# Performance work log

Measured on AMD Instinct MI355X. Metric: run time of the kernel, lower is better.

The kernel has to match this reference:

```python
import jax, jax.numpy as jnp
import numpy as np

INPUT_DIM = 32
HIDDEN = 64
BATCH = 4096
SEQ = 256


def _uniform(key, shape, bound):
    return jax.random.uniform(key, shape, dtype=jnp.float32, minval=-bound, maxval=bound)


def setup_inputs() -> dict:
    key = jax.random.key(0)
    ks = jax.random.split(key, 16)
    kb = 1.0 / np.sqrt(HIDDEN)  # torch LSTM/Linear init bound
    x = jax.random.normal(ks[0], (BATCH, SEQ, INPUT_DIM), dtype=jnp.float32)
    # LSTM layer 0 (input_dim -> hidden), gate order i,f,g,o stacked on dim 0
    Wih0 = _uniform(ks[1], (4 * HIDDEN, INPUT_DIM), kb)
    Whh0 = _uniform(ks[2], (4 * HIDDEN, HIDDEN), kb)
    bih0 = _uniform(ks[3], (4 * HIDDEN,), kb)
    bhh0 = _uniform(ks[4], (4 * HIDDEN,), kb)
    # LSTM layer 1 (hidden -> hidden)
    Wih1 = _uniform(ks[5], (4 * HIDDEN, HIDDEN), kb)
    Whh1 = _uniform(ks[6], (4 * HIDDEN, HIDDEN), kb)
    bih1 = _uniform(ks[7], (4 * HIDDEN,), kb)
    bhh1 = _uniform(ks[8], (4 * HIDDEN,), kb)
    # MLP head
    W1 = _uniform(ks[9], (HIDDEN, HIDDEN), kb)
    b1 = _uniform(ks[10], (HIDDEN,), kb)
    W2 = _uniform(ks[11], (1, HIDDEN), kb)
    b2 = _uniform(ks[12], (1,), kb)
    return {"x": x, "Wih0": Wih0, "Whh0": Whh0, "bih0": bih0, "bhh0": bhh0,
            "Wih1": Wih1, "Whh1": Whh1, "bih1": bih1, "bhh1": bhh1,
            "W1": W1, "b1": b1, "W2": W2, "b2": b2}


def lstm_layer(x, Wih, Whh, bih, bhh):
    """x: [B,T,D] -> hidden sequence [B,T,H]. PyTorch gate order i,f,g,o."""
    B = x.shape[0]
    H = Whh.shape[1]
    # precompute input contribution for all timesteps: [B,T,4H]
    gx = jnp.einsum('btd,gd->btg', x, Wih) + bih + bhh

    def step(carry, g_t):
        h, c = carry
        g = g_t + h @ Whh.T  # [B,4H]
        i, f, gg, o = jnp.split(g, 4, axis=-1)
        i = jax.nn.sigmoid(i)
        f = jax.nn.sigmoid(f)
        gg = jnp.tanh(gg)
        o = jax.nn.sigmoid(o)
        c = f * c + i * gg
        h = o * jnp.tanh(c)
        return (h, c), h

    h0 = jnp.zeros((B, H), x.dtype)
    c0 = jnp.zeros((B, H), x.dtype)
    _, hs = jax.lax.scan(step, (h0, c0), jnp.swapaxes(gx, 0, 1))  # hs: [T,B,H]
    return jnp.swapaxes(hs, 0, 1)


def reference(x, Wih0, Whh0, bih0, bhh0, Wih1, Whh1, bih1, bhh1, W1, b1, W2, b2):
    h1 = lstm_layer(x, Wih0, Whh0, bih0, bhh0)    # [B,T,H]
    h2 = lstm_layer(h1, Wih1, Whh1, bih1, bhh1)   # [B,T,H]
    last = h2[:, -1, :]                            # [B,H]
    f = jax.nn.relu(last @ W1.T + b1)              # dropout = identity (eval)
    out = f @ W2.T + b2                            # [B,1]
    return out
```

## Files before the change

kernel.cpp:

```cpp
#include <hip/hip_runtime.h>
#include <cstdint>

typedef __attribute__((ext_vector_type(8))) _Float16 f16x8;
typedef __attribute__((ext_vector_type(4))) float f32x4;

#define SEQL 256

#define WS_B0H   0
#define WS_B0L   49152
#define WS_B1H   98304
#define WS_BIAS0 229376
#define WS_BIAS1 230400

#define ASTR 656
#define L_A  0
#define L_HD 10496
#define HDSTR 272
#define LDS_TOTAL 14848

#define NEG_L   -1.4426950408889634f
#define NEG_2L  -2.8853900817779268f
#define LO_SCALE 2048.0f
#define LO_INV   4.8828125e-4f

__device__ __forceinline__ float ex2(float x) { return __builtin_amdgcn_exp2f(x); }
__device__ __forceinline__ float rcp_(float x) { return __builtin_amdgcn_rcpf(x); }
__device__ __forceinline__ float sig_s(float vs) { return rcp_(1.f + ex2(vs)); }
__device__ __forceinline__ float tanh_s(float vs) {
  float e = ex2(-fabsf(vs));
  float r = (1.f - e) * rcp_(1.f + e);
  return copysignf(r, -vs);
}
__device__ __forceinline__ float tanh_c(float c) {
  float e = ex2(fabsf(c) * NEG_2L);
  float r = (1.f - e) * rcp_(1.f + e);
  return copysignf(r, c);
}
__device__ __forceinline__ f32x4 mfma16(f16x8 a, f16x8 b, f32x4 c) {
  return __builtin_amdgcn_mfma_f32_16x16x32_f16(a, b, c, 0, 0, 0);
}
__device__ __forceinline__ f16x8 zero8() {
  f16x8 z;
#pragma unroll
  for (int i = 0; i < 8; ++i) z[i] = (_Float16)0.f;
  return z;
}
template <int PAT>
__device__ __forceinline__ int dppq(int v) {
  return __builtin_amdgcn_update_dpp(v, v, PAT, 0xf, 0xf, true);
}
__device__ __forceinline__ void quad_transpose(float (&v)[4], bool lodd, bool l2b) {
  int a0 = __float_as_int(v[0]), a1 = __float_as_int(v[1]);
  int a2 = __float_as_int(v[2]), a3 = __float_as_int(v[3]);
  int d0 = dppq<0xB1>(a0), d1 = dppq<0xB1>(a1);
  int d2 = dppq<0xB1>(a2), d3 = dppq<0xB1>(a3);
  int x0 = lodd ? d1 : a0;
  int x1 = lodd ? a1 : d0;
  int x2 = lodd ? d3 : a2;
  int x3 = lodd ? a3 : d2;
  int e0 = dppq<0x4E>(x0), e1 = dppq<0x4E>(x1);
  int e2 = dppq<0x4E>(x2), e3 = dppq<0x4E>(x3);
  v[0] = __int_as_float(l2b ? e2 : x0);
  v[1] = __int_as_float(l2b ? e3 : x1);
  v[2] = __int_as_float(l2b ? x2 : e0);
  v[3] = __int_as_float(l2b ? x3 : e1);
}

__global__ __launch_bounds__(256) void prep(
    const float* __restrict__ Wih0, const float* __restrict__ Whh0,
    const float* __restrict__ bih0, const float* __restrict__ bhh0,
    const float* __restrict__ Wih1, const float* __restrict__ Whh1,
    const float* __restrict__ bih1, const float* __restrict__ bhh1,
    unsigned char* __restrict__ ws) {
  int e = blockIdx.x * 256 + threadIdx.x;
  if (e < 24576) {
    int j = e & 7, lane = (e >> 3) & 63, nt = (e >> 9) & 15, ks = e >> 13;
    int kdim = ks * 32 + (lane >> 4) * 8 + j;
    int col = nt * 16 + (lane & 15);
    int ko = col >> 2, g = col & 3;
    float w = (kdim < 32) ? Wih0[(g * 64 + ko) * 32 + kdim]
                          : Whh0[(g * 64 + ko) * 64 + (kdim - 32)];
    w *= (g == 2) ? NEG_2L : NEG_L;
    _Float16 hi = (_Float16)w;
    _Float16 lo = (_Float16)((w - (float)hi) * LO_SCALE);
    ((_Float16*)(ws + WS_B0H))[e] = hi;
    ((_Float16*)(ws + WS_B0L))[e] = lo;
  } else if (e < 57344) {
    int r = e - 24576;
    int j = r & 7, lane = (r >> 3) & 63, nt = (r >> 9) & 15, ks = r >> 13;
    int kdim = ks * 32 + (lane >> 4) * 8 + j;
    int col = nt * 16 + (lane & 15);
    int ko = col >> 2, g = col & 3;
    float w = (kdim < 64) ? Wih1[(g * 64 + ko) * 64 + kdim]
                          : Whh1[(g * 64 + ko) * 64 + (kdim - 64)];
    w *= (g == 2) ? NEG_2L : NEG_L;
    _Float16 hi = (_Float16)w;
    _Float16 lo = (_Float16)((w - (float)hi) * LO_SCALE);
    ((_Float16*)(ws + WS_B1H))[r] = hi;
    ((_Float16*)(ws + WS_B1H + 65536))[r] = lo;
  } else if (e < 57856) {
    int r = e - 57344;
    int col = r & 255, ko = col >> 2, g = col & 3;
    float v = (r < 256) ? bih0[g * 64 + ko] + bhh0[g * 64 + ko]
                        : bih1[g * 64 + ko] + bhh1[g * 64 + ko];
    v *= (g == 2) ? NEG_2L : NEG_L;
    ((float*)(ws + (r < 256 ? WS_BIAS0 : WS_BIAS1)))[col] = v;
  }
}

__global__ __launch_bounds__(1024, 4) void lstm_mfma5(
    const float* __restrict__ x, const unsigned char* __restrict__ ws,
    const float* __restrict__ W1, const float* __restrict__ b1,
    const float* __restrict__ W2, const float* __restrict__ b2,
    float* __restrict__ out) {
  __shared__ __align__(16) unsigned char lds[LDS_TOTAL];
  const int tid = threadIdx.x;
  const int lane = tid & 63, wave = tid >> 6;
  const int q = lane >> 4, mcol = lane & 15;
  const bool lodd = (lane & 1) != 0, l2b = (lane & 2) != 0;

  f16x8 b0h[3], b0l[3], b1h[4], b1l[4];
#pragma unroll
  for (int ks = 0; ks < 3; ++ks) {
    int rec = (ks * 16 + wave) * 64 + lane;
    b0h[ks] = ((const f16x8*)(ws + WS_B0H))[rec];
    b0l[ks] = ((const f16x8*)(ws + WS_B0L))[rec];
  }
#pragma unroll
  for (int ks = 0; ks < 4; ++ks) {
    int rec = (ks * 16 + wave) * 64 + lane;
    b1h[ks] = ((const f16x8*)(ws + WS_B1H))[rec];
    b1l[ks] = ((const f16x8*)(ws + WS_B1H + 65536))[rec];
  }
  const int col = wave * 16 + mcol;
  const float bias0r = ((const float*)(ws + WS_BIAS0))[col];
  const float bias1r = ((const float*)(ws + WS_BIAS1))[col];

  for (int i = tid; i < 2624; i += 1024) ((unsigned*)(lds + L_A))[i] = 0u;

  const bool do_x = tid < 512;
  const int bx = tid >> 5, d = tid & 31;
  const float* xcol = x + (size_t)(blockIdx.x * 16 + (do_x ? bx : 0)) * (SEQL * 32) + d;
  if (do_x) {
    *(_Float16*)(lds + L_A + bx * ASTR + d * 2) = (_Float16)xcol[0];
  }
  const int brow = q * 4 + (lane & 3);
  const int kc = wave * 4 + (mcol >> 2);
  float c1 = 0.f, c2 = 0.f, h2f = 0.f;
  f16x8 ah1[2];
  ah1[0] = ah1[1] = zero8();
  __syncthreads();

  auto step = [&](int t, const int par) {
    const int xrd = par * 64, xwr = (par ^ 1) * 64;
    const int h1s = 128 + par * 128;
    const int h2rd = 384 + (par ^ 1) * 128;
    const int h2wr = 384 + par * 128;

    float xnext = 0.f;
    if (do_x && t < SEQL - 1) xnext = xcol[(t + 1) * 32];

    f16x8 ax = *(const f16x8*)(lds + L_A + mcol * ASTR + xrd + q * 16);
    f32x4 accH, accL;
    accH[0] = accH[1] = accH[2] = accH[3] = bias0r;
    accL[0] = accL[1] = accL[2] = accL[3] = 0.f;
    accH = mfma16(ax, b0h[0], accH);
    accL = mfma16(ax, b0l[0], accL);
#pragma unroll
    for (int ks = 0; ks < 2; ++ks) {
      accH = mfma16(ah1[ks], b0h[ks + 1], accH);
      accL = mfma16(ah1[ks], b0l[ks + 1], accL);
    }
    {
      float g4[4];
#pragma unroll
      for (int i = 0; i < 4; ++i) g4[i] = fmaf(accL[i], LO_INV, accH[i]);
      quad_transpose(g4, lodd, l2b);
      float gi = sig_s(g4[0]), gf = sig_s(g4[1]);
      float gg = tanh_s(g4[2]), go = sig_s(g4[3]);
      c1 = fmaf(gf, c1, gi * gg);
      float h = go * tanh_c(c1);
      *(_Float16*)(lds + L_A + brow * ASTR + h1s + kc * 2) = (_Float16)h;
    }
    if (do_x && t < SEQL - 1) {
      *(_Float16*)(lds + L_A + bx * ASTR + xwr + d * 2) = (_Float16)xnext;
    }
    __syncthreads();

#pragma unroll
    for (int ks = 0; ks < 2; ++ks)
      ah1[ks] = *(const f16x8*)(lds + L_A + mcol * ASTR + h1s + ks * 64 + q * 16);
    f16x8 h2fr[2];
#pragma unroll
    for (int ks = 0; ks < 2; ++ks)
      h2fr[ks] = *(const f16x8*)(lds + L_A + mcol * ASTR + h2rd + ks * 64 + q * 16);
    accH[0] = accH[1] = accH[2] = accH[3] = bias1r;
    accL[0] = accL[1] = accL[2] = accL[3] = 0.f;
#pragma unroll
    for (int ks = 0; ks < 2; ++ks) {
      accH = mfma16(ah1[ks], b1h[ks], accH);
      accL = mfma16(ah1[ks], b1l[ks], accL);
    }
#pragma unroll
    for (int ks = 0; ks < 2; ++ks) {
      accH = mfma16(h2fr[ks], b1h[ks + 2], accH);
      accL = mfma16(h2fr[ks], b1l[ks + 2], accL);
    }
    {
      float g4[4];
#pragma unroll
      for (int i = 0; i < 4; ++i) g4[i] = fmaf(accL[i], LO_INV, accH[i]);
      quad_transpose(g4, lodd, l2b);
      float gi = sig_s(g4[0]), gf = sig_s(g4[1]);
      float gg = tanh_s(g4[2]), go = sig_s(g4[3]);
      c2 = fmaf(gf, c2, gi * gg);
      float h = go * tanh_c(c2);
      h2f = h;
      *(_Float16*)(lds + L_A + brow * ASTR + h2wr + kc * 2) = (_Float16)h;
    }
  };

#pragma unroll 1
  for (int tp = 0; tp < SEQL / 2; ++tp) {
    step(2 * tp, 0);
    step(2 * tp + 1, 1);
  }

  __syncthreads();
  *(float*)(lds + L_HD + brow * HDSTR + kc * 4) = h2f;
  __syncthreads();
  if (tid < 256) {
    const int s = tid & 15, bo = tid >> 4;
    const float* h2row = (const float*)(lds + L_HD + bo * HDSTR);
    float partial = 0.f;
#pragma unroll
    for (int kk4 = 0; kk4 < 4; ++kk4) {
      int kk = s * 4 + kk4;
      float f = b1[kk];
#pragma unroll
      for (int j = 0; j < 64; j += 4) {
        f32x4 w = *(const f32x4*)(W1 + kk * 64 + j);
        f = fmaf(w[0], h2row[j], f);
        f = fmaf(w[1], h2row[j + 1], f);
        f = fmaf(w[2], h2row[j + 2], f);
        f = fmaf(w[3], h2row[j + 3], f);
      }
      f = fmaxf(f, 0.f);
      partial = fmaf(f, W2[kk], partial);
    }
    partial += __shfl_xor(partial, 8, 64);
    partial += __shfl_xor(partial, 4, 64);
    partial += __shfl_xor(partial, 2, 64);
    partial += __shfl_xor(partial, 1, 64);
    if (s == 0) out[blockIdx.x * 16 + bo] = partial + b2[0];
  }
}

extern "C" void kernel_launch(void* const* d_in, const int* in_sizes, int n_in,
                              void* d_out, int out_size, void* d_ws, size_t ws_size,
                              hipStream_t stream) {
  const float* x    = (const float*)d_in[0];
  const float* Wih0 = (const float*)d_in[1];
  const float* Whh0 = (const float*)d_in[2];
  const float* bih0 = (const float*)d_in[3];
  const float* bhh0 = (const float*)d_in[4];
  const float* Wih1 = (const float*)d_in[5];
  const float* Whh1 = (const float*)d_in[6];
  const float* bih1 = (const float*)d_in[7];
  const float* bhh1 = (const float*)d_in[8];
  const float* W1   = (const float*)d_in[9];
  const float* b1   = (const float*)d_in[10];
  const float* W2   = (const float*)d_in[11];
  const float* b2   = (const float*)d_in[12];
  unsigned char* ws = (unsigned char*)d_ws;
  float* out = (float*)d_out;

  prep<<<(57856 + 255) / 256, 256, 0, stream>>>(Wih0, Whh0, bih0, bhh0,
                                                Wih1, Whh1, bih1, bhh1, ws);
  lstm_mfma5<<<256, 1024, 0, stream>>>(x, ws, W1, b1, W2, b2, out);
}
```

Measured before the change: 488.1 us.

## Wavefront-skew LSTM layers and swap MFMA operands to drop quad transpose

Layer 2 now runs one timestep behind layer 1, so both layers' MFMAs and cell updates share one iteration and one barrier per timestep instead of two. The MFMA operands are swapped so each lane directly holds the four gates of one hidden unit, which removes the DPP quad transpose. The tanh activations are rewritten as 2*sigmoid-1. This adds a prologue and epilogue step and keeps extra h2 fragments live in registers. The 2*sigmoid-1 form may lose some precision near zero.

```diff
diff --git a/kernel.cpp b/kernel.cpp
--- a/kernel.cpp
+++ b/kernel.cpp
@@ -25,17 +25,6 @@
 
 __device__ __forceinline__ float ex2(float x) { return __builtin_amdgcn_exp2f(x); }
 __device__ __forceinline__ float rcp_(float x) { return __builtin_amdgcn_rcpf(x); }
-__device__ __forceinline__ float sig_s(float vs) { return rcp_(1.f + ex2(vs)); }
-__device__ __forceinline__ float tanh_s(float vs) {
-  float e = ex2(-fabsf(vs));
-  float r = (1.f - e) * rcp_(1.f + e);
-  return copysignf(r, -vs);
-}
-__device__ __forceinline__ float tanh_c(float c) {
-  float e = ex2(fabsf(c) * NEG_2L);
-  float r = (1.f - e) * rcp_(1.f + e);
-  return copysignf(r, c);
-}
 __device__ __forceinline__ f32x4 mfma16(f16x8 a, f16x8 b, f32x4 c) {
   return __builtin_amdgcn_mfma_f32_16x16x32_f16(a, b, c, 0, 0, 0);
 }
@@ -44,26 +33,6 @@
 #pragma unroll
   for (int i = 0; i < 8; ++i) z[i] = (_Float16)0.f;
   return z;
-}
-template <int PAT>
-__device__ __forceinline__ int dppq(int v) {
-  return __builtin_amdgcn_update_dpp(v, v, PAT, 0xf, 0xf, true);
-}
-__device__ __forceinline__ void quad_transpose(float (&v)[4], bool lodd, bool l2b) {
-  int a0 = __float_as_int(v[0]), a1 = __float_as_int(v[1]);
-  int a2 = __float_as_int(v[2]), a3 = __float_as_int(v[3]);
-  int d0 = dppq<0xB1>(a0), d1 = dppq<0xB1>(a1);
-  int d2 = dppq<0xB1>(a2), d3 = dppq<0xB1>(a3);
-  int x0 = lodd ? d1 : a0;
-  int x1 = lodd ? a1 : d0;
-  int x2 = lodd ? d3 : a2;
-  int x3 = lodd ? a3 : d2;
-  int e0 = dppq<0x4E>(x0), e1 = dppq<0x4E>(x1);
-  int e2 = dppq<0x4E>(x2), e3 = dppq<0x4E>(x3);
-  v[0] = __int_as_float(l2b ? e2 : x0);
-  v[1] = __int_as_float(l2b ? e3 : x1);
-  v[2] = __int_as_float(l2b ? x2 : e0);
-  v[3] = __int_as_float(l2b ? x3 : e1);
 }
 
 __global__ __launch_bounds__(256) void prep(
@@ -108,7 +77,7 @@
   }
 }
 
-__global__ __launch_bounds__(1024, 4) void lstm_mfma5(
+__global__ __launch_bounds__(1024, 4) void lstm_mfma6(
     const float* __restrict__ x, const unsigned char* __restrict__ ws,
     const float* __restrict__ W1, const float* __restrict__ b1,
     const float* __restrict__ W2, const float* __restrict__ b2,
@@ -116,8 +85,7 @@
   __shared__ __align__(16) unsigned char lds[LDS_TOTAL];
   const int tid = threadIdx.x;
   const int lane = tid & 63, wave = tid >> 6;
-  const int q = lane >> 4, mcol = lane & 15;
-  const bool lodd = (lane & 1) != 0, l2b = (lane & 2) != 0;
+  const int q = lane >> 4, bcol = lane & 15;
 
   f16x8 b0h[3], b0l[3], b1h[4], b1l[4];
 #pragma unroll
@@ -132,9 +100,10 @@
     b1h[ks] = ((const f16x8*)(ws + WS_B1H))[rec];
     b1l[ks] = ((const f16x8*)(ws + WS_B1H + 65536))[rec];
   }
-  const int col = wave * 16 + mcol;
-  const float bias0r = ((const float*)(ws + WS_BIAS0))[col];
-  const float bias1r = ((const float*)(ws + WS_BIAS1))[col];
+  const f32x4 bias0v = ((const f32x4*)(ws + WS_BIAS0))[wave * 4 + q];
+  const f32x4 bias1v = ((const f32x4*)(ws + WS_BIAS1))[wave * 4 + q];
+  f32x4 z4;
+  z4[0] = z4[1] = z4[2] = z4[3] = 0.f;
 
   for (int i = tid; i < 2624; i += 1024) ((unsigned*)(lds + L_A))[i] = 0u;
 
@@ -144,90 +113,90 @@
   if (do_x) {
     *(_Float16*)(lds + L_A + bx * ASTR + d * 2) = (_Float16)xcol[0];
   }
-  const int brow = q * 4 + (lane & 3);
-  const int kc = wave * 4 + (mcol >> 2);
+
+  const int ard = bcol * ASTR + q * 16;
+  const int hwr = bcol * ASTR + (wave * 4 + q) * 2;
+
   float c1 = 0.f, c2 = 0.f, h2f = 0.f;
-  f16x8 ah1[2];
-  ah1[0] = ah1[1] = zero8();
+  f16x8 ah1[2], ah2[2], ax;
+  ah1[0] = ah1[1] = ah2[0] = ah2[1] = zero8();
   __syncthreads();
-
-  auto step = [&](int t, const int par) {
-    const int xrd = par * 64, xwr = (par ^ 1) * 64;
+  ax = *(const f16x8*)(lds + L_A + ard + 0);
+
+  auto cell = [&](const f32x4& aH, const f32x4& aL, float& c) -> float {
+    float p0 = fmaf(aL[0], LO_INV, aH[0]);
+    float p1 = fmaf(aL[1], LO_INV, aH[1]);
+    float p2 = fmaf(aL[2], LO_INV, aH[2]);
+    float p3 = fmaf(aL[3], LO_INV, aH[3]);
+    float gi = rcp_(1.f + ex2(p0));
+    float gf = rcp_(1.f + ex2(p1));
+    float gg = fmaf(2.f, rcp_(1.f + ex2(p2)), -1.f);
+    float go = rcp_(1.f + ex2(p3));
+    c = fmaf(gf, c, gi * gg);
+    float tc = fmaf(2.f, rcp_(1.f + ex2(c * NEG_2L)), -1.f);
+    return go * tc;
+  };
+
+  auto iter = [&](int t, int par, bool doL2) {
     const int h1s = 128 + par * 128;
-    const int h2rd = 384 + (par ^ 1) * 128;
-    const int h2wr = 384 + par * 128;
-
+    const int h2s = 384 + par * 128;
+    const int xwr = (par ^ 1) * 64;
     float xnext = 0.f;
     if (do_x && t < SEQL - 1) xnext = xcol[(t + 1) * 32];
 
-    f16x8 ax = *(const f16x8*)(lds + L_A + mcol * ASTR + xrd + q * 16);
-    f32x4 accH, accL;
-    accH[0] = accH[1] = accH[2] = accH[3] = bias0r;
-    accL[0] = accL[1] = accL[2] = accL[3] = 0.f;
-    accH = mfma16(ax, b0h[0], accH);
-    accL = mfma16(ax, b0l[0], accL);
+    f32x4 aH0 = mfma16(b0h[0], ax, bias0v);
+    f32x4 aL0 = mfma16(b0l[0], ax, z4);
+    f32x4 aH1 = mfma16(b1h[0], ah1[0], bias1v);
+    f32x4 aL1 = mfma16(b1l[0], ah1[0], z4);
+    aH1 = mfma16(b1h[1], ah1[1], aH1);
+    aL1 = mfma16(b1l[1], ah1[1], aL1);
 #pragma unroll
     for (int ks = 0; ks < 2; ++ks) {
-      accH = mfma16(ah1[ks], b0h[ks + 1], accH);
-      accL = mfma16(ah1[ks], b0l[ks + 1], accL);
-    }
-    {
-      float g4[4];
-#pragma unroll
-      for (int i = 0; i < 4; ++i) g4[i] = fmaf(accL[i], LO_INV, accH[i]);
-      quad_transpose(g4, lodd, l2b);
-      float gi = sig_s(g4[0]), gf = sig_s(g4[1]);
-      float gg = tanh_s(g4[2]), go = sig_s(g4[3]);
-      c1 = fmaf(gf, c1, gi * gg);
-      float h = go * tanh_c(c1);
-      *(_Float16*)(lds + L_A + brow * ASTR + h1s + kc * 2) = (_Float16)h;
+      aH0 = mfma16(b0h[ks + 1], ah1[ks], aH0);
+      aL0 = mfma16(b0l[ks + 1], ah1[ks], aL0);
+      aH1 = mfma16(b1h[ks + 2], ah2[ks], aH1);
+      aL1 = mfma16(b1l[ks + 2], ah2[ks], aL1);
+    }
+    float h1 = cell(aH0, aL0, c1);
+    *(_Float16*)(lds + L_A + hwr + h1s) = (_Float16)h1;
+    if (doL2) {
+      float h2 = cell(aH1, aL1, c2);
+      *(_Float16*)(lds + L_A + hwr + h2s) = (_Float16)h2;
     }
     if (do_x && t < SEQL - 1) {
       *(_Float16*)(lds + L_A + bx * ASTR + xwr + d * 2) = (_Float16)xnext;
     }
     __syncthreads();
-
-#pragma unroll
-    for (int ks = 0; ks < 2; ++ks)
-      ah1[ks] = *(const f16x8*)(lds + L_A + mcol * ASTR + h1s + ks * 64 + q * 16);
-    f16x8 h2fr[2];
-#pragma unroll
-    for (int ks = 0; ks < 2; ++ks)
-      h2fr[ks] = *(const f16x8*)(lds + L_A + mcol * ASTR + h2rd + ks * 64 + q * 16);
-    accH[0] = accH[1] = accH[2] = accH[3] = bias1r;
-    accL[0] = accL[1] = accL[2] = accL[3] = 0.f;
+    ah1[0] = *(const f16x8*)(lds + L_A + ard + h1s);
+    ah1[1] = *(const f16x8*)(lds + L_A + ard + h1s + 64);
+    ah2[0] = *(const f16x8*)(lds + L_A + ard + h2s);
+    ah2[1] = *(const f16x8*)(lds + L_A + ard + h2s + 64);
+    ax     = *(const f16x8*)(lds + L_A + ard + xwr);
+  };
+
+  iter(0, 0, false);
+#pragma unroll 1
+  for (int tp = 0; tp < 127; ++tp) {
+    iter(2 * tp + 1, 1, true);
+    iter(2 * tp + 2, 0, true);
+  }
+  iter(255, 1, true);
+
+  {
+    f32x4 aH = mfma16(b1h[0], ah1[0], bias1v);
+    f32x4 aL = mfma16(b1l[0], ah1[0], z4);
+    aH = mfma16(b1h[1], ah1[1], aH);
+    aL = mfma16(b1l[1], ah1[1], aL);
 #pragma unroll
     for (int ks = 0; ks < 2; ++ks) {
-      accH = mfma16(ah1[ks], b1h[ks], accH);
-      accL = mfma16(ah1[ks], b1l[ks], accL);
-    }
-#pragma unroll
-    for (int ks = 0; ks < 2; ++ks) {
-      accH = mfma16(h2fr[ks], b1h[ks + 2], accH);
-      accL = mfma16(h2fr[ks], b1l[ks + 2], accL);
-    }
-    {
-      float g4[4];
-#pragma unroll
-      for (int i = 0; i < 4; ++i) g4[i] = fmaf(accL[i], LO_INV, accH[i]);
-      quad_transpose(g4, lodd, l2b);
-      float gi = sig_s(g4[0]), gf = sig_s(g4[1]);
-      float gg = tanh_s(g4[2]), go = sig_s(g4[3]);
-      c2 = fmaf(gf, c2, gi * gg);
-      float h = go * tanh_c(c2);
-      h2f = h;
-      *(_Float16*)(lds + L_A + brow * ASTR + h2wr + kc * 2) = (_Float16)h;
-    }
-  };
-
-#pragma unroll 1
-  for (int tp = 0; tp < SEQL / 2; ++tp) {
-    step(2 * tp, 0);
-    step(2 * tp + 1, 1);
+      aH = mfma16(b1h[ks + 2], ah2[ks], aH);
+      aL = mfma16(b1l[ks + 2], ah2[ks], aL);
+    }
+    h2f = cell(aH, aL, c2);
   }
 
   __syncthreads();
-  *(float*)(lds + L_HD + brow * HDSTR + kc * 4) = h2f;
+  *(float*)(lds + L_HD + bcol * HDSTR + (wave * 4 + q) * 4) = h2f;
   __syncthreads();
   if (tid < 256) {
     const int s = tid & 15, bo = tid >> 4;
@@ -277,5 +246,5 @@
 
   prep<<<(57856 + 255) / 256, 256, 0, stream>>>(Wih0, Whh0, bih0, bhh0,
                                                 Wih1, Whh1, bih1, bhh1, ws);
-  lstm_mfma5<<<256, 1024, 0, stream>>>(x, ws, W1, b1, W2, b2, out);
-}
+  lstm_mfma6<<<256, 1024, 0, stream>>>(x, ws, W1, b1, W2, b2, out);
+}
```

New measurement: 442.9 us. -9.3%, faster.
